# Kernel tuning notes

Measured on AMD Instinct MI355X. Metric: run time of the kernel, lower is better.

Reference implementation:

```python
import jax, jax.numpy as jnp
import numpy as np

N, H, R2, T, E, POS, L = 50000, 256, 460, 3, 100000, 3, 2
RRELU_SLOPE = (1.0 / 8 + 1.0 / 3) / 2  # eval-mode rrelu = leaky with mean slope


def setup_inputs() -> dict:
    key = jax.random.key(0)
    ks = jax.random.split(key, 24)
    s = 0.05
    return {
        'src': jax.random.randint(ks[0], (T, E), 0, N, dtype=jnp.int32),
        'dst': jax.random.randint(ks[1], (T, E), 0, N, dtype=jnp.int32),
        'etype': jax.random.randint(ks[2], (T, E), 0, R2, dtype=jnp.int32),
        'r_to_e': jax.random.randint(ks[3], (T, E), 0, N, dtype=jnp.int32),
        'r_seg': jax.random.randint(ks[4], (T, E), 0, R2, dtype=jnp.int32),
        'pos_enc': jax.random.normal(ks[5], (T, N, POS), jnp.float32),
        'dynamic_emb': jax.random.normal(ks[6], (N, H), jnp.float32),
        'emb_rel': jax.random.normal(ks[7], (R2, H), jnp.float32) * s,
        'gru_W_ih': jax.random.normal(ks[8], (3 * H, 2 * H), jnp.float32) * s,
        'gru_W_hh': jax.random.normal(ks[9], (3 * H, H), jnp.float32) * s,
        'gru_b_ih': jnp.zeros((3 * H,), jnp.float32),
        'gru_b_hh': jnp.zeros((3 * H,), jnp.float32),
        'W_neigh': jax.random.normal(ks[10], (L, H, H), jnp.float32) * s,
        'W_loop': jax.random.normal(ks[11], (L, H, H), jnp.float32) * s,
        'W_evolve': jax.random.normal(ks[12], (L, H, H), jnp.float32) * s,
        'W_hp': jax.random.normal(ks[13], (H, H + POS), jnp.float32) * s,
        'b_hp': jnp.zeros((H,), jnp.float32),
        'W_v': jax.random.normal(ks[14], (H, H), jnp.float32) * s,
        'b_v': jnp.zeros((H,), jnp.float32),
        'W_o': jax.random.normal(ks[15], (H, H), jnp.float32) * s,
        'b_o': jnp.zeros((H,), jnp.float32),
        'time_W': jax.random.normal(ks[16], (H, H), jnp.float32) * s,
        'time_b': jnp.zeros((H,), jnp.float32),
        'glob_W': jax.random.normal(ks[17], (H, H), jnp.float32) * s,
        'glob_b': jnp.zeros((H,), jnp.float32),
    }


def _l2norm(x):
    return x / jnp.maximum(jnp.linalg.norm(x, axis=-1, keepdims=True), 1e-12)


def _gru_cell(x, hprev, W_ih, W_hh, b_ih, b_hh):
    gi = x @ W_ih.T + b_ih
    gh = hprev @ W_hh.T + b_hh
    i_r, i_z, i_n = jnp.split(gi, 3, axis=-1)
    h_r, h_z, h_n = jnp.split(gh, 3, axis=-1)
    r = jax.nn.sigmoid(i_r + h_r)
    z = jax.nn.sigmoid(i_z + h_z)
    n = jnp.tanh(i_n + r * h_n)
    return (1.0 - z) * n + z * hprev


def _forward(src, dst, etype, r_to_e, r_seg, pos_enc, dynamic_emb, emb_rel,
             gru_W_ih, gru_W_hh, gru_b_ih, gru_b_hh,
             W_neigh, W_loop, W_evolve, W_hp, b_hp, W_v, b_v, W_o, b_o,
             time_W, time_b, glob_W, glob_b):
    h = _l2norm(dynamic_emb)  # layer_norm=True path: F.normalize
    h0 = emb_rel
    outs = []
    for t in range(T):  # sequence_len snapshots
        # per-relation mean of involved entity embeddings (r_len/uniq_r spans)
        feat = h[r_to_e[t]]                                   # [E, H]
        sums = jax.ops.segment_sum(feat, r_seg[t], num_segments=R2)
        cnts = jax.ops.segment_sum(jnp.ones((E,), feat.dtype), r_seg[t], num_segments=R2)
        x_mean = jnp.where(cnts[:, None] > 0, sums / jnp.maximum(cnts, 1.0)[:, None], 0.0)
        x_in = jnp.concatenate([emb_rel, x_mean], axis=1)     # [R2, 2H]
        h0 = _l2norm(_gru_cell(x_in, h0, gru_W_ih, gru_W_hh, gru_b_ih, gru_b_hh))
        # UnionRGCN layers: msg = (h_src + rel[etype]) @ W_neigh, sum-agg * 1/in_deg,
        # plus self-loop (loop_weight if in_deg>0 else evolve_loop_weight), rrelu.
        deg = jax.ops.segment_sum(jnp.ones((E,), h.dtype), dst[t], num_segments=N)
        norm = jnp.where(deg > 0, 1.0 / jnp.maximum(deg, 1.0), 0.0)[:, None]
        nh = h
        for l in range(L):
            msg = (nh[src[t]] + h0[etype[t]]) @ W_neigh[l]    # [E, H]
            agg = jax.ops.segment_sum(msg, dst[t], num_segments=N) * norm
            loop = jnp.where(deg[:, None] > 0, nh @ W_loop[l], nh @ W_evolve[l])
            pre = agg + loop
            nh = jnp.where(pre >= 0, pre, RRELU_SLOPE * pre)
        current_h = nh
        # global attention over seq-len-1 -> out_proj(v_proj(x)) in eval mode
        atten_in = jnp.tanh(jnp.concatenate([current_h, pos_enc[t]], axis=1) @ W_hp.T + b_hp)
        global_h = (atten_in @ W_v.T + b_v) @ W_o.T + b_o
        current_h = _l2norm(current_h)
        tw = jax.nn.sigmoid(h @ time_W + time_b)
        h = tw * current_h + (1.0 - tw) * h
        gw = jax.nn.sigmoid(h @ glob_W + glob_b)
        outs.append(gw * global_h + (1.0 - gw) * h)
    return jnp.stack(outs)  # [T, N, H] history_embs


def reference(src, dst, etype, r_to_e, r_seg, pos_enc, dynamic_emb, emb_rel,
              gru_W_ih, gru_W_hh, gru_b_ih, gru_b_hh,
              W_neigh, W_loop, W_evolve, W_hp, b_hp, W_v, b_v, W_o, b_o,
              time_W, time_b, glob_W, glob_b):
    return _forward(src, dst, etype, r_to_e, r_seg, pos_enc, dynamic_emb, emb_rel,
                    gru_W_ih, gru_W_hh, gru_b_ih, gru_b_hh,
                    W_neigh, W_loop, W_evolve, W_hp, b_hp, W_v, b_v, W_o, b_o,
                    time_W, time_b, glob_W, glob_b)
```

## Files before the change

### kernel.cpp

```cpp
#include <hip/hip_runtime.h>
#include <math.h>

#define NN 50000
#define HH 256
#define RR 460
#define TT 3
#define EE 100000
#define PP 3
#define SLOPE 0.22916666666666666f
#define NBIN (RR + NN)
#define NBIN3 (3*NBIN)

typedef __bf16 bf16_t;
typedef bf16_t bf16x8 __attribute__((ext_vector_type(8)));
typedef float f32x4 __attribute__((ext_vector_type(4)));

static const size_t NHf = (size_t)NN * HH;

__device__ __forceinline__ float sigm(float x){ return 1.0f/(1.0f+__expf(-x)); }
__device__ __forceinline__ float leaky(float x){ return (x >= 0.f) ? x : SLOPE*x; }

__device__ __forceinline__ void gload_lds16(const void* g, void* l){
  __builtin_amdgcn_global_load_lds((const __attribute__((address_space(1))) void*)g,
                                   (__attribute__((address_space(3))) void*)l, 16, 0, 0);
}

__global__ __launch_bounds__(256) void tconv_all_k(
    const float* __restrict__ Wn, const float* __restrict__ Wl, const float* __restrict__ We,
    const float* __restrict__ timW, const float* __restrict__ globW,
    bf16_t* __restrict__ bst2, bf16_t* __restrict__ wdT,
    bf16_t* __restrict__ timT, bf16_t* __restrict__ globT){
  int z = blockIdx.z;
  const float* in; const float* in2 = nullptr; bf16_t* outp; int ldout;
  switch(z){
    case 0: in = Wn;           outp = bst2;                       ldout = 512; break;
    case 1: in = Wl;           outp = bst2 + 256;                 ldout = 512; break;
    case 2: in = Wn + 65536;   outp = bst2 + (size_t)256*512;     ldout = 512; break;
    case 3: in = Wl + 65536;   outp = bst2 + (size_t)256*512+256; ldout = 512; break;
    case 4: in = We;          in2 = Wl;         outp = wdT;         ldout = 256; break;
    case 5: in = We + 65536;  in2 = Wl + 65536; outp = wdT + 65536; ldout = 256; break;
    case 6: in = timW;  outp = timT;  ldout = 256; break;
    default:in = globW; outp = globT; ldout = 256; break;
  }
  __shared__ float tile[32][33];
  int n0 = blockIdx.x*32, k0 = blockIdx.y*32;
  int tx = threadIdx.x & 31, ty = threadIdx.x >> 5;
  #pragma unroll
  for (int j=0;j<4;j++){
    size_t idx = (size_t)(k0+ty+j*8)*256 + n0+tx;
    float v = in[idx];
    if (in2) v -= in2[idx];
    tile[ty+j*8][tx] = v;
  }
  __syncthreads();
  #pragma unroll
  for (int j=0;j<4;j++)
    outp[(size_t)(n0+ty+j*8)*ldout + k0+tx] = (bf16_t)tile[tx][ty+j*8];
}

__global__ __launch_bounds__(256) void copyall_k(const float* __restrict__ gW_ih,
    const float* __restrict__ gW_hh, const float* __restrict__ W_hp, const float* __restrict__ emb_rel,
    bf16_t* __restrict__ wihAT, bf16_t* __restrict__ wihBT, bf16_t* __restrict__ whhT,
    bf16_t* __restrict__ whpT, bf16_t* __restrict__ h0b){
  int r = blockIdx.x, c = threadIdx.x, y = blockIdx.y;
  if (y == 0)      wihAT[(size_t)r*256+c] = (bf16_t)gW_ih[(size_t)r*512 + c];
  else if (y == 1) wihBT[(size_t)r*256+c] = (bf16_t)gW_ih[(size_t)r*512 + 256 + c];
  else if (y == 2) whhT[(size_t)r*256+c]  = (bf16_t)gW_hh[(size_t)r*256 + c];
  else if (y == 3){ if (r < 256) whpT[(size_t)r*256+c] = (bf16_t)W_hp[(size_t)r*259 + c]; }
  else            { if (r < RR)  h0b[(size_t)r*256+c]  = (bf16_t)emb_rel[(size_t)r*256 + c]; }
}

__global__ __launch_bounds__(256) void misc_k(const float* __restrict__ W_hp, float* __restrict__ WP,
    const float* __restrict__ W_o, const float* __restrict__ b_v, const float* __restrict__ b_o,
    float* __restrict__ b_ov){
  if (blockIdx.x == 0){
    int j = threadIdx.x;
    #pragma unroll
    for (int p=0;p<PP;p++) WP[p*HH + j] = W_hp[(size_t)j*259 + HH + p];
  } else {
    int n = threadIdx.x;
    float s = b_o[n];
    for (int j=0;j<256;j++) s += W_o[(size_t)n*256+j]*b_v[j];
    b_ov[n] = s;
  }
}

__global__ __launch_bounds__(256) void copy_bfw_k(const float* __restrict__ in, bf16_t* __restrict__ outp){
  int r = blockIdx.x, c = threadIdx.x;
  outp[(size_t)r*HH + c] = (bf16_t)in[(size_t)r*HH + c];
}

__global__ __launch_bounds__(256) void sgemm_k(const float* __restrict__ A, const float* __restrict__ B,
                                               float* __restrict__ C, int M, int N, int K){
  __shared__ float As[16][128];
  __shared__ float Bs[16][64];
  int tid = threadIdx.x;
  int tx = tid & 15, ty = tid >> 4;
  int rowBase = blockIdx.x * 128;
  int colBase = blockIdx.y * 64;
  float acc[8][4];
  #pragma unroll
  for (int i=0;i<8;i++)
    #pragma unroll
    for (int j=0;j<4;j++) acc[i][j]=0.f;
  for (int k0=0;k0<K;k0+=16){
    #pragma unroll
    for (int ss=0; ss<2; ss++){
      int s = tid + ss*256;
      int r = s >> 2;
      int kk = (s & 3)*4;
      float4 v = make_float4(0.f,0.f,0.f,0.f);
      int grow = rowBase + r;
      if (grow < M) v = *(const float4*)(A + (size_t)grow*K + k0 + kk);
      As[kk+0][r]=v.x; As[kk+1][r]=v.y; As[kk+2][r]=v.z; As[kk+3][r]=v.w;
    }
    {
      int r = tid >> 4, cc = (tid & 15)*4;
      float4 v = *(const float4*)(B + (size_t)(k0+r)*N + colBase + cc);
      *(float4*)&Bs[r][cc] = v;
    }
    __syncthreads();
    #pragma unroll
    for (int kk=0;kk<16;kk++){
      float a[8], b[4];
      *(float4*)&a[0] = *(const float4*)&As[kk][ty*8];
      *(float4*)&a[4] = *(const float4*)&As[kk][ty*8+4];
      *(float4*)&b[0] = *(const float4*)&Bs[kk][tx*4];
      #pragma unroll
      for (int i=0;i<8;i++)
        #pragma unroll
        for (int j=0;j<4;j++)
          acc[i][j] = fmaf(a[i], b[j], acc[i][j]);
    }
    __syncthreads();
  }
  #pragma unroll
  for (int i=0;i<8;i++){
    int gr = rowBase + ty*8 + i;
    if (gr >= M) continue;
    float4 v = make_float4(acc[i][0], acc[i][1], acc[i][2], acc[i][3]);
    *(float4*)(C + (size_t)gr*N + colBase + tx*4) = v;
  }
}

template<int EPI, int HASB>
__global__ __launch_bounds__(256) void mgemm_k(
    const bf16_t* __restrict__ A0, const bf16_t* __restrict__ Bt,
    float* __restrict__ C, const float* __restrict__ bias,
    int M, int N, int K, const float* __restrict__ e1){
  __shared__ bf16_t As[128*64];
  __shared__ bf16_t Bs[128*64];
  int tid = threadIdx.x;
  int lane = tid & 63, w = tid >> 6;
  int wm = w >> 1, wn = w & 1;
  int rowBase = blockIdx.x * 128;
  int colBase = blockIdx.y * 128;
  f32x4 acc[4][4] = {};

  int lrow = lane >> 3;
  int p    = lane & 7;
  int arow[4];
  #pragma unroll
  for (int c = 0; c < 4; c++){
    int gr = rowBase + c*32 + w*8 + lrow;
    arow[c] = min(gr, M-1);
  }
  for (int k0 = 0; k0 < K; k0 += 64){
    #pragma unroll
    for (int c = 0; c < 4; c++){
      int r = c*32 + w*8 + lrow;
      int s = p ^ (r & 7);
      gload_lds16(A0 + (size_t)arow[c]*K + k0 + s*8, As + (size_t)(c*32 + w*8)*64);
      int gb = colBase + r;
      gload_lds16(Bt + (size_t)gb*K + k0 + s*8, Bs + (size_t)(c*32 + w*8)*64);
    }
    asm volatile("s_waitcnt vmcnt(0)" ::: "memory");
    __syncthreads();
    #pragma unroll
    for (int kk = 0; kk < 2; kk++){
      bf16x8 af[4], bfr[4];
      int sg = kk*4 + (lane >> 4);
      #pragma unroll
      for (int i = 0; i < 4; i++){
        int r = wm*64 + i*16 + (lane & 15);
        af[i] = *(const bf16x8*)(As + r*64 + (sg ^ (r & 7))*8);
      }
      #pragma unroll
      for (int j = 0; j < 4; j++){
        int rn = wn*64 + j*16 + (lane & 15);
        bfr[j] = *(const bf16x8*)(Bs + rn*64 + (sg ^ (rn & 7))*8);
      }
      #pragma unroll
      for (int i = 0; i < 4; i++)
        #pragma unroll
        for (int j = 0; j < 4; j++)
          acc[i][j] = __builtin_amdgcn_mfma_f32_16x16x32_bf16(af[i], bfr[j], acc[i][j], 0, 0, 0);
    }
    __syncthreads();
  }
  int colv[4]; float bb[4];
  #pragma unroll
  for (int j = 0; j < 4; j++){
    colv[j] = colBase + wn*64 + j*16 + (lane & 15);
    bb[j] = HASB ? bias[colv[j]] : 0.f;
  }
  #pragma unroll
  for (int i = 0; i < 4; i++){
    #pragma unroll
    for (int q = 0; q < 4; q++){
      int grt = rowBase + wm*64 + i*16 + ((lane >> 4) << 2) + q;
      if (grt >= M) continue;
      #pragma unroll
      for (int j = 0; j < 4; j++){
        size_t idx = (size_t)grt*N + colv[j];
        float v = acc[i][j][q] + bb[j];
        if (EPI == 8) v += e1[idx];
        C[idx] = v;
      }
    }
  }
}

template<int EPI, int WF32, int WBF, int HASB, int SPLITA>
__global__ __launch_bounds__(512) void mgemm2_k(
    const bf16_t* __restrict__ A0, const bf16_t* __restrict__ A1,
    const bf16_t* __restrict__ Bt,
    float* __restrict__ C, bf16_t* __restrict__ Cb, const float* __restrict__ bias,
    int M, int K,
    const float* __restrict__ e1, const float* __restrict__ e2,
    const bf16_t* __restrict__ eb, const bf16_t* __restrict__ eb2,
    const int* __restrict__ degp, const int* __restrict__ z, const int* __restrict__ nzp){
  int rowBase = blockIdx.x * 128;
  int nzv = 0;
  if (EPI == 5){
    nzv = nzp[0];
    if (rowBase >= nzv) return;
  }
  __shared__ bf16_t As[128*64];
  __shared__ bf16_t Bs[256*64];
  int tid = threadIdx.x;
  int lane = tid & 63, w = tid >> 6;
  int wm = w >> 2, wn = w & 3;
  f32x4 acc[4][4] = {};

  int lrow8 = lane >> 3;
  int p     = lane & 7;
  int arow[2];
  #pragma unroll
  for (int c = 0; c < 2; c++){
    int r = w*16 + c*8 + lrow8;
    int gr = rowBase + r;
    if (EPI == 5) arow[c] = z[min(gr, nzv-1)];
    else          arow[c] = min(gr, M-1);
  }
  for (int k0 = 0; k0 < K; k0 += 64){
    const bf16_t* Ap; int koff; size_t lda;
    if (SPLITA){ Ap = (k0 < 256) ? A0 : A1; koff = k0 & 255; lda = 256; }
    else       { Ap = A0; koff = k0; lda = (size_t)K; }
    #pragma unroll
    for (int c = 0; c < 2; c++){
      int r = w*16 + c*8 + lrow8;
      int s = p ^ (r & 7);
      gload_lds16(Ap + (size_t)arow[c]*lda + koff + s*8, As + (size_t)(w*16 + c*8)*64);
    }
    #pragma unroll
    for (int c = 0; c < 4; c++){
      int r = w*32 + c*8 + lrow8;
      int s = p ^ (r & 7);
      gload_lds16(Bt + (size_t)r*K + k0 + s*8, Bs + (size_t)(w*32 + c*8)*64);
    }
    asm volatile("s_waitcnt vmcnt(0)" ::: "memory");
    __syncthreads();
    #pragma unroll
    for (int kk = 0; kk < 2; kk++){
      bf16x8 af[4], bfr[4];
      int sg = kk*4 + (lane >> 4);
      #pragma unroll
      for (int i = 0; i < 4; i++){
        int r = wm*64 + i*16 + (lane & 15);
        af[i] = *(const bf16x8*)(As + r*64 + (sg ^ (r & 7))*8);
      }
      #pragma unroll
      for (int j = 0; j < 4; j++){
        int rn = wn*64 + j*16 + (lane & 15);
        bfr[j] = *(const bf16x8*)(Bs + rn*64 + (sg ^ (rn & 7))*8);
      }
      #pragma unroll
      for (int i = 0; i < 4; i++)
        #pragma unroll
        for (int j = 0; j < 4; j++)
          acc[i][j] = __builtin_amdgcn_mfma_f32_16x16x32_bf16(af[i], bfr[j], acc[i][j], 0, 0, 0);
    }
    __syncthreads();
  }
  int colv[4]; float bb[4], wp0[4], wp1[4], wp2[4];
  #pragma unroll
  for (int j = 0; j < 4; j++){
    colv[j] = wn*64 + j*16 + (lane & 15);
    bb[j] = HASB ? bias[colv[j]] : 0.f;
    if (EPI == 2){ wp0[j] = e2[colv[j]]; wp1[j] = e2[256+colv[j]]; wp2[j] = e2[512+colv[j]]; }
  }
  #pragma unroll
  for (int i = 0; i < 4; i++){
    #pragma unroll
    for (int q = 0; q < 4; q++){
      int grt = rowBase + wm*64 + i*16 + ((lane >> 4) << 2) + q;
      if (EPI == 5){ if (grt >= nzv) continue; }
      else         { if (grt >= M) continue; }
      int orow = (EPI == 5) ? z[grt] : grt;
      int dflag = 0;
      if (EPI == 4) dflag = degp[orow];
      float p0=0.f, p1=0.f, p2=0.f;
      if (EPI == 2){ p0 = e1[(size_t)grt*3]; p1 = e1[(size_t)grt*3+1]; p2 = e1[(size_t)grt*3+2]; }
      #pragma unroll
      for (int j = 0; j < 4; j++){
        size_t idx = (size_t)orow*256 + colv[j];
        float v = acc[i][j][q] + bb[j];
        if (EPI == 2) v = tanhf(v + p0*wp0[j] + p1*wp1[j] + p2*wp2[j]);
        if (EPI == 3){
          float g = sigm(v);
          v = g*(float)eb[idx] + (1.f-g)*(float)eb2[idx];
        }
        if (EPI == 4) v = (dflag > 0) ? leaky(v) : v;
        if (EPI == 5){
          float praw = (float)Cb[idx];
          v = leaky(praw + v);
        }
        if (EPI == 7) v = sigm(v);
        if (WF32) C[idx] = v;
        if (WBF)  Cb[idx] = (bf16_t)v;
      }
    }
  }
}

__global__ __launch_bounds__(256) void l2norm_k(const float* __restrict__ in, bf16_t* __restrict__ outb){
  int i = blockIdx.x, c = threadIdx.x;
  size_t idx = (size_t)i*HH + c;
  float v = in[idx];
  float ss = v*v;
  #pragma unroll
  for (int o=32;o;o>>=1) ss += __shfl_down(ss, o);
  __shared__ float red[4];
  if ((threadIdx.x & 63)==0) red[threadIdx.x>>6] = ss;
  __syncthreads();
  float tot = red[0]+red[1]+red[2]+red[3];
  outb[idx] = (bf16_t)(v / fmaxf(sqrtf(tot), 1e-12f));
}

__global__ __launch_bounds__(256) void hist3_k(const int* __restrict__ r_seg, const int* __restrict__ dst,
                                               int* __restrict__ cnt){
  int q = blockIdx.x*256 + threadIdx.x;
  if (q >= 3*2*EE) return;
  int t = q / (2*EE);
  int e = q - t*2*EE;
  if (e < EE) atomicAdd(cnt + t*NBIN + r_seg[(size_t)t*EE + e], 1);
  else        atomicAdd(cnt + t*NBIN + RR + dst[(size_t)t*EE + (e-EE)], 1);
}

__global__ __launch_bounds__(1024) void scan1_k(const int* __restrict__ cnt, int* __restrict__ start,
                                                int* __restrict__ bsum, int n){
  __shared__ int s[1024];
  int t = blockIdx.x*1024 + threadIdx.x;
  int v = (t < n) ? cnt[t] : 0;
  s[threadIdx.x] = v;
  __syncthreads();
  for (int off = 1; off < 1024; off <<= 1){
    int x = (threadIdx.x >= off) ? s[threadIdx.x - off] : 0;
    __syncthreads();
    s[threadIdx.x] += x;
    __syncthreads();
  }
  if (t < n) start[t] = s[threadIdx.x] - v;
  if (threadIdx.x == 1023) bsum[blockIdx.x] = s[1023];
}
__global__ __launch_bounds__(256) void scan2_k(const int* __restrict__ bsum, int* __restrict__ boff,
                                               int* __restrict__ start, int nb, int n){
  __shared__ int s[256];
  int t = threadIdx.x;
  int v = (t < nb) ? bsum[t] : 0;
  s[t] = v;
  __syncthreads();
  for (int off = 1; off < 256; off <<= 1){
    int x = (t >= off) ? s[t-off] : 0;
    __syncthreads();
    s[t] += x;
    __syncthreads();
  }
  if (t < nb) boff[t] = s[t] - v;
  if (t == 255) start[n] = s[255];
}
__global__ __launch_bounds__(1024) void scan3_k(int* __restrict__ start, int* __restrict__ cur,
                                                const int* __restrict__ boff, int n){
  int t = blockIdx.x*1024 + threadIdx.x;
  if (t < n){
    int v = start[t] + boff[blockIdx.x];
    start[t] = v;
    cur[t] = v;
  }
}

__global__ __launch_bounds__(256) void fill3_k(const int* __restrict__ r_seg, const int* __restrict__ r_to_e,
    const int* __restrict__ dst, const int* __restrict__ src, const int* __restrict__ ety,
    int* __restrict__ cur, int* __restrict__ rnode, unsigned* __restrict__ dpack){
  int q = blockIdx.x*256 + threadIdx.x;
  if (q >= 3*2*EE) return;
  int t = q / (2*EE);
  int e = q - t*2*EE;
  if (e < EE){
    size_t ge = (size_t)t*EE + e;
    int pp = atomicAdd(cur + t*NBIN + r_seg[ge], 1);
    rnode[pp - EE*t] = r_to_e[ge];
  } else {
    size_t ge = (size_t)t*EE + (e - EE);
    int pp = atomicAdd(cur + t*NBIN + RR + dst[ge], 1);
    dpack[pp - EE*(t+1)] = (unsigned)src[ge] | ((unsigned)ety[ge] << 16);
  }
}

__global__ __launch_bounds__(256) void compact3_k(const int* __restrict__ cnt, int* __restrict__ zAll,
                                                  int* __restrict__ nz){
  int q = blockIdx.x*256 + threadIdx.x;
  int lane = threadIdx.x & 63;
  bool valid = q < 3*NN;
  int qc = valid ? q : 3*NN - 1;
  int t = qc / NN, d = qc - t*NN;
  bool pred = valid && (cnt[t*NBIN + RR + d] == 0);
  int tA = __shfl(t, 0), tB = __shfl(t, 63);
  if (tA == tB){
    unsigned long long m = __ballot(pred);
    int total = __popcll(m);
    int base = 0;
    if (lane == 0 && total > 0) base = atomicAdd(nz + tA, total);
    base = __shfl(base, 0);
    if (pred){
      int myoff = __popcll(m & ((1ULL << lane) - 1ULL));
      zAll[(size_t)tA*NN + base + myoff] = d;
    }
  } else {
    if (pred){
      int pp = atomicAdd(nz + t, 1);
      zAll[(size_t)t*NN + pp] = d;
    }
  }
}

__global__ __launch_bounds__(256) void rmean_k(const int* __restrict__ startT, const int* __restrict__ rnode,
    const bf16_t* __restrict__ hb, bf16_t* __restrict__ meanb, int rbase){
  int r = blockIdx.x, c = threadIdx.x;
  int s0 = startT[r] - rbase, s1 = startT[r+1] - rbase;
  float acc = 0.f, acc2 = 0.f;
  int i = s0;
  for (; i + 1 < s1; i += 2){
    acc  += (float)hb[(size_t)rnode[i]*HH + c];
    acc2 += (float)hb[(size_t)rnode[i+1]*HH + c];
  }
  if (i < s1) acc += (float)hb[(size_t)rnode[i]*HH + c];
  acc += acc2;
  int cnt = s1 - s0;
  meanb[(size_t)r*HH + c] = (bf16_t)((cnt > 0) ? acc/(float)cnt : 0.f);
}

__global__ __launch_bounds__(256) void gru_gate_k(const float* __restrict__ gi,
    const float* __restrict__ ghb, float* __restrict__ h0, bf16_t* __restrict__ h0b){
  int r = blockIdx.x, c = threadIdx.x;
  float ir = gi[(size_t)r*768 + c],       hr = ghb[(size_t)r*768 + c];
  float iz = gi[(size_t)r*768 + 256 + c], hz = ghb[(size_t)r*768 + 256 + c];
  float in_ = gi[(size_t)r*768 + 512 + c], hn = ghb[(size_t)r*768 + 512 + c];
  float rg = sigm(ir + hr);
  float z  = sigm(iz + hz);
  float n  = tanhf(in_ + rg*hn);
  float hp = h0[(size_t)r*HH + c];
  float v = (1.f - z)*n + z*hp;
  float ss = v*v;
  #pragma unroll
  for (int o=32;o;o>>=1) ss += __shfl_down(ss, o);
  __shared__ float red[4];
  if ((threadIdx.x & 63)==0) red[threadIdx.x>>6] = ss;
  __syncthreads();
  float tot = red[0]+red[1]+red[2]+red[3];
  float nv = v / fmaxf(sqrtf(tot), 1e-12f);
  h0[(size_t)r*HH + c] = nv;
  h0b[(size_t)r*HH + c] = (bf16_t)nv;
}

__global__ __launch_bounds__(256) void gatherM_k(const bf16_t* __restrict__ nin,
    const bf16_t* __restrict__ h0b, const int* __restrict__ startT,
    const unsigned* __restrict__ dpack, bf16_t* __restrict__ Amean, int ebase){
  int w = threadIdx.x >> 6, ln = threadIdx.x & 63;
  int d = blockIdx.x*4 + w;
  if (d >= NN) return;
  int s0 = startT[RR + d] - ebase, s1 = startT[RR + d + 1] - ebase;
  int deg = s1 - s0;
  float a0=0.f, a1=0.f, a2=0.f, a3=0.f;
  for (int i = s0; i < s1; i++){
    unsigned se = dpack[i];
    int s = (int)(se & 0xffffu);
    int r = (int)(se >> 16);
    uint2 ra = *(const uint2*)(nin + (size_t)s*HH + ln*4);
    uint2 rb = *(const uint2*)(h0b + (size_t)r*HH + ln*4);
    a0 += __uint_as_float((ra.x & 0xffffu) << 16) + __uint_as_float((rb.x & 0xffffu) << 16);
    a1 += __uint_as_float(ra.x & 0xffff0000u)     + __uint_as_float(rb.x & 0xffff0000u);
    a2 += __uint_as_float((ra.y & 0xffffu) << 16) + __uint_as_float((rb.y & 0xffffu) << 16);
    a3 += __uint_as_float(ra.y & 0xffff0000u)     + __uint_as_float(rb.y & 0xffff0000u);
  }
  float inv = (deg > 0) ? 1.f/(float)deg : 0.f;
  bf16_t m[4] = { (bf16_t)(a0*inv), (bf16_t)(a1*inv), (bf16_t)(a2*inv), (bf16_t)(a3*inv) };
  *(uint2*)(Amean + (size_t)d*HH + ln*4) = *(const uint2*)m;
}

__global__ __launch_bounds__(256) void l2up_k(const bf16_t* __restrict__ nh2b, const bf16_t* __restrict__ sg,
    bf16_t* __restrict__ hb){
  int i = blockIdx.x, c = threadIdx.x;
  size_t idx = (size_t)i*HH + c;
  float v = (float)nh2b[idx];
  float ss = v*v;
  #pragma unroll
  for (int o=32;o;o>>=1) ss += __shfl_down(ss, o);
  __shared__ float red[4];
  if ((threadIdx.x & 63)==0) red[threadIdx.x>>6] = ss;
  __syncthreads();
  float tot = red[0]+red[1]+red[2]+red[3];
  float curn = v / fmaxf(sqrtf(tot), 1e-12f);
  float s = (float)sg[idx];
  float hn = s*curn + (1.f-s)*(float)hb[idx];
  hb[idx] = (bf16_t)hn;
}

extern "C" void kernel_launch(void* const* d_in, const int* in_sizes, int n_in,
                              void* d_out, int out_size, void* d_ws, size_t ws_size,
                              hipStream_t stream) {
  const int*   src     = (const int*)  d_in[0];
  const int*   dst     = (const int*)  d_in[1];
  const int*   etype   = (const int*)  d_in[2];
  const int*   r_to_e  = (const int*)  d_in[3];
  const int*   r_seg   = (const int*)  d_in[4];
  const float* pos_enc = (const float*)d_in[5];
  const float* dyn_emb = (const float*)d_in[6];
  const float* emb_rel = (const float*)d_in[7];
  const float* gW_ih   = (const float*)d_in[8];
  const float* gW_hh   = (const float*)d_in[9];
  const float* gb_ih   = (const float*)d_in[10];
  const float* gb_hh   = (const float*)d_in[11];
  const float* W_neigh = (const float*)d_in[12];
  const float* W_loop  = (const float*)d_in[13];
  const float* W_evolve= (const float*)d_in[14];
  const float* W_hp    = (const float*)d_in[15];
  const float* b_hp    = (const float*)d_in[16];
  const float* W_v     = (const float*)d_in[17];
  const float* b_v     = (const float*)d_in[18];
  const float* W_o     = (const float*)d_in[19];
  const float* b_o     = (const float*)d_in[20];
  const float* time_W  = (const float*)d_in[21];
  const float* time_b  = (const float*)d_in[22];
  const float* glob_W  = (const float*)d_in[23];
  const float* glob_b  = (const float*)d_in[24];
  float* out = (float*)d_out;
  (void)in_sizes; (void)n_in; (void)out_size; (void)ws_size;

  char* ws = (char*)d_ws;
  size_t off = 0;
  auto allocB = [&](size_t bytes)->char*{
    char* pp = ws + off; off += (bytes + 255) & ~(size_t)255;
    return pp;
  };
  float*  tmp    = (float*) allocB(NHf*4);
  bf16_t* h_bf   = (bf16_t*)allocB(NHf*2);
  bf16_t* nh_bf  = (bf16_t*)allocB(NHf*2);
  bf16_t* nh2_bf = (bf16_t*)allocB(NHf*2);
  bf16_t* gh_bf  = (bf16_t*)allocB(NHf*2);
  bf16_t* Amean  = (bf16_t*)tmp;
  bf16_t* sgate  = (bf16_t*)(tmp + NHf/2);
  bf16_t* attn_bf= nh_bf;

  float*  h0    = (float*) allocB((size_t)RR*HH*4);
  bf16_t* h0b   = (bf16_t*)allocB((size_t)RR*HH*2);
  bf16_t* meanb = (bf16_t*)allocB((size_t)RR*HH*2);
  float*  gi0   = (float*) allocB((size_t)RR*768*4);
  float*  gi    = (float*) allocB((size_t)RR*768*4);
  float*  ghb   = (float*) allocB((size_t)RR*768*4);
  bf16_t* wihAT = (bf16_t*)allocB((size_t)768*256*2);
  bf16_t* wihBT = (bf16_t*)allocB((size_t)768*256*2);
  bf16_t* whhT  = (bf16_t*)allocB((size_t)768*256*2);
  float*  WP    = (float*) allocB((size_t)PP*HH*4);
  float*  WovF  = (float*) allocB((size_t)HH*HH*4);
  float*  b_ov  = (float*) allocB((size_t)HH*4);
  bf16_t* bst2  = (bf16_t*)allocB((size_t)2*HH*512*2);
  bf16_t* wdT   = (bf16_t*)allocB((size_t)2*HH*HH*2);
  bf16_t* whpT  = (bf16_t*)allocB((size_t)HH*HH*2);
  bf16_t* wovT  = (bf16_t*)allocB((size_t)HH*HH*2);
  bf16_t* timT  = (bf16_t*)allocB((size_t)HH*HH*2);
  bf16_t* globT = (bf16_t*)allocB((size_t)HH*HH*2);
  int* cnt    = (int*)allocB((size_t)(NBIN3+4)*4);
  int* start  = (int*)allocB((size_t)(NBIN3+1)*4);
  int* cur    = (int*)allocB((size_t)NBIN3*4);
  int* rnode  = (int*)allocB((size_t)3*EE*4);
  unsigned* dpack = (unsigned*)allocB((size_t)3*EE*4);
  int* zAll   = (int*)allocB((size_t)3*NN*4);
  int* bsum   = (int*)allocB(256*4);
  int* boff   = (int*)allocB(256*4);
  int* nz     = cnt + NBIN3;

  const int MT  = (NN + 127)/128;
  const int NB3 = (NBIN3 + 1023)/1024;

  copyall_k<<<dim3(768,5), 256, 0, stream>>>(gW_ih, gW_hh, W_hp, emb_rel,
                                             wihAT, wihBT, whhT, whpT, h0b);
  tconv_all_k<<<dim3(8,8,8), 256, 0, stream>>>(W_neigh, W_loop, W_evolve, time_W, glob_W,
                                               bst2, wdT, timT, globT);
  misc_k<<<2, 256, 0, stream>>>(W_hp, WP, W_o, b_v, b_o, b_ov);
  sgemm_k<<<dim3(2,4), 256, 0, stream>>>(W_o, W_v, WovF, 256, 256, 256);
  copy_bfw_k<<<HH, 256, 0, stream>>>(WovF, wovT);
  l2norm_k<<<NN, 256, 0, stream>>>(dyn_emb, h_bf);
  hipMemcpyAsync(h0, emb_rel, (size_t)RR*HH*4, hipMemcpyDeviceToDevice, stream);
  mgemm_k<0,1><<<dim3(4,6), 256, 0, stream>>>(h0b, wihAT, gi0, gb_ih, RR, 768, 256, nullptr);

  hipMemsetAsync(cnt, 0, (size_t)(NBIN3+4)*4, stream);
  hist3_k<<<(6*EE+255)/256, 256, 0, stream>>>(r_seg, dst, cnt);
  scan1_k<<<NB3, 1024, 0, stream>>>(cnt, start, bsum, NBIN3);
  scan2_k<<<1, 256, 0, stream>>>(bsum, boff, start, NB3, NBIN3);
  scan3_k<<<NB3, 1024, 0, stream>>>(start, cur, boff, NBIN3);
  fill3_k<<<(6*EE+255)/256, 256, 0, stream>>>(r_seg, r_to_e, dst, src, etype, cur, rnode, dpack);
  compact3_k<<<(3*NN+255)/256, 256, 0, stream>>>(cnt, zAll, nz);

  for (int t=0; t<TT; t++){
    const float* posT = pos_enc + (size_t)t*NN*PP;
    const int* startT = start + (size_t)t*NBIN;
    const int* degT   = cnt + (size_t)t*NBIN + RR;
    const int* zT     = zAll + (size_t)t*NN;
    const int* nzT    = nz + t;

    rmean_k<<<RR, 256, 0, stream>>>(startT, rnode, h_bf, meanb, EE*t);
    mgemm_k<8,0><<<dim3(4,6), 256, 0, stream>>>(meanb, wihBT, gi, nullptr, RR, 768, 256, gi0);
    mgemm_k<0,1><<<dim3(4,6), 256, 0, stream>>>(h0b, whhT, ghb, gb_hh, RR, 768, 256, nullptr);
    gru_gate_k<<<RR, 256, 0, stream>>>(gi, ghb, h0, h0b);

    gatherM_k<<<(NN+3)/4, 256, 0, stream>>>(h_bf, h0b, startT, dpack, Amean, EE*(t+1));
    mgemm2_k<4,0,1,0,1><<<MT, 512, 0, stream>>>(Amean, h_bf, bst2, nullptr, nh_bf, nullptr,
        NN, 512, nullptr, nullptr, nullptr, nullptr, degT, nullptr, nullptr);
    mgemm2_k<5,0,1,0,0><<<MT, 512, 0, stream>>>(h_bf, nullptr, wdT, nullptr, nh_bf, nullptr,
        NN, 256, nullptr, nullptr, nullptr, nullptr, nullptr, zT, nzT);

    gatherM_k<<<(NN+3)/4, 256, 0, stream>>>(nh_bf, h0b, startT, dpack, Amean, EE*(t+1));
    mgemm2_k<4,0,1,0,1><<<MT, 512, 0, stream>>>(Amean, nh_bf, bst2 + (size_t)HH*512, nullptr, nh2_bf, nullptr,
        NN, 512, nullptr, nullptr, nullptr, nullptr, degT, nullptr, nullptr);
    mgemm2_k<5,0,1,0,0><<<MT, 512, 0, stream>>>(nh_bf, nullptr, wdT + (size_t)HH*HH, nullptr, nh2_bf, nullptr,
        NN, 256, nullptr, nullptr, nullptr, nullptr, nullptr, zT, nzT);

    mgemm2_k<2,0,1,1,0><<<MT, 512, 0, stream>>>(nh2_bf, nullptr, whpT, nullptr, attn_bf, b_hp,
        NN, 256, posT, WP, nullptr, nullptr, nullptr, nullptr, nullptr);
    mgemm2_k<0,0,1,1,0><<<MT, 512, 0, stream>>>(attn_bf, nullptr, wovT, nullptr, gh_bf, b_ov,
        NN, 256, nullptr, nullptr, nullptr, nullptr, nullptr, nullptr, nullptr);

    mgemm2_k<7,0,1,1,0><<<MT, 512, 0, stream>>>(h_bf, nullptr, timT, nullptr, sgate, time_b,
        NN, 256, nullptr, nullptr, nullptr, nullptr, nullptr, nullptr, nullptr);
    l2up_k<<<NN, 256, 0, stream>>>(nh2_bf, sgate, h_bf);
    mgemm2_k<3,1,0,1,0><<<MT, 512, 0, stream>>>(h_bf, nullptr, globT, out + (size_t)t*NHf, nullptr, glob_b,
        NN, 256, nullptr, nullptr, gh_bf, h_bf, nullptr, nullptr, nullptr);
  }
}
```

Measured before the change: 1.370 ms.

## Halve GEMM row tile to 64 and unroll gather loop by two

New measurement: 1.329 ms. 3.0% less time.

```diff
diff --git a/kernel.cpp b/kernel.cpp
--- a/kernel.cpp
+++ b/kernel.cpp
@@ -222,7 +222,7 @@
 }
 
 template<int EPI, int WF32, int WBF, int HASB, int SPLITA>
-__global__ __launch_bounds__(512) void mgemm2_k(
+__global__ __launch_bounds__(512, 6) void mgemm2_k(
     const bf16_t* __restrict__ A0, const bf16_t* __restrict__ A1,
     const bf16_t* __restrict__ Bt,
     float* __restrict__ C, bf16_t* __restrict__ Cb, const float* __restrict__ bias,
@@ -230,38 +230,35 @@
     const float* __restrict__ e1, const float* __restrict__ e2,
     const bf16_t* __restrict__ eb, const bf16_t* __restrict__ eb2,
     const int* __restrict__ degp, const int* __restrict__ z, const int* __restrict__ nzp){
-  int rowBase = blockIdx.x * 128;
+  int rowBase = blockIdx.x * 64;
   int nzv = 0;
   if (EPI == 5){
     nzv = nzp[0];
     if (rowBase >= nzv) return;
   }
-  __shared__ bf16_t As[128*64];
+  __shared__ bf16_t As[64*64];
   __shared__ bf16_t Bs[256*64];
   int tid = threadIdx.x;
   int lane = tid & 63, w = tid >> 6;
-  int wm = w >> 2, wn = w & 3;
-  f32x4 acc[4][4] = {};
+  f32x4 acc[4][2] = {};
 
   int lrow8 = lane >> 3;
   int p     = lane & 7;
-  int arow[2];
-  #pragma unroll
-  for (int c = 0; c < 2; c++){
-    int r = w*16 + c*8 + lrow8;
+  int arow;
+  {
+    int r = w*8 + lrow8;
     int gr = rowBase + r;
-    if (EPI == 5) arow[c] = z[min(gr, nzv-1)];
-    else          arow[c] = min(gr, M-1);
+    if (EPI == 5) arow = z[min(gr, nzv-1)];
+    else          arow = min(gr, M-1);
   }
   for (int k0 = 0; k0 < K; k0 += 64){
     const bf16_t* Ap; int koff; size_t lda;
     if (SPLITA){ Ap = (k0 < 256) ? A0 : A1; koff = k0 & 255; lda = 256; }
     else       { Ap = A0; koff = k0; lda = (size_t)K; }
-    #pragma unroll
-    for (int c = 0; c < 2; c++){
-      int r = w*16 + c*8 + lrow8;
+    {
+      int r = w*8 + lrow8;
       int s = p ^ (r & 7);
-      gload_lds16(Ap + (size_t)arow[c]*lda + koff + s*8, As + (size_t)(w*16 + c*8)*64);
+      gload_lds16(Ap + (size_t)arow*lda + koff + s*8, As + (size_t)(w*8)*64);
     }
     #pragma unroll
     for (int c = 0; c < 4; c++){
@@ -273,30 +270,30 @@
     __syncthreads();
     #pragma unroll
     for (int kk = 0; kk < 2; kk++){
-      bf16x8 af[4], bfr[4];
+      bf16x8 af[4], bfr[2];
       int sg = kk*4 + (lane >> 4);
       #pragma unroll
       for (int i = 0; i < 4; i++){
-        int r = wm*64 + i*16 + (lane & 15);
+        int r = i*16 + (lane & 15);
         af[i] = *(const bf16x8*)(As + r*64 + (sg ^ (r & 7))*8);
       }
       #pragma unroll
-      for (int j = 0; j < 4; j++){
-        int rn = wn*64 + j*16 + (lane & 15);
+      for (int j = 0; j < 2; j++){
+        int rn = w*32 + j*16 + (lane & 15);
         bfr[j] = *(const bf16x8*)(Bs + rn*64 + (sg ^ (rn & 7))*8);
       }
       #pragma unroll
       for (int i = 0; i < 4; i++)
         #pragma unroll
-        for (int j = 0; j < 4; j++)
+        for (int j = 0; j < 2; j++)
           acc[i][j] = __builtin_amdgcn_mfma_f32_16x16x32_bf16(af[i], bfr[j], acc[i][j], 0, 0, 0);
     }
     __syncthreads();
   }
-  int colv[4]; float bb[4], wp0[4], wp1[4], wp2[4];
-  #pragma unroll
-  for (int j = 0; j < 4; j++){
-    colv[j] = wn*64 + j*16 + (lane & 15);
+  int colv[2]; float bb[2], wp0[2], wp1[2], wp2[2];
+  #pragma unroll
+  for (int j = 0; j < 2; j++){
+    colv[j] = w*32 + j*16 + (lane & 15);
     bb[j] = HASB ? bias[colv[j]] : 0.f;
     if (EPI == 2){ wp0[j] = e2[colv[j]]; wp1[j] = e2[256+colv[j]]; wp2[j] = e2[512+colv[j]]; }
   }
@@ -304,7 +301,7 @@
   for (int i = 0; i < 4; i++){
     #pragma unroll
     for (int q = 0; q < 4; q++){
-      int grt = rowBase + wm*64 + i*16 + ((lane >> 4) << 2) + q;
+      int grt = rowBase + i*16 + ((lane >> 4) << 2) + q;
       if (EPI == 5){ if (grt >= nzv) continue; }
       else         { if (grt >= M) continue; }
       int orow = (EPI == 5) ? z[grt] : grt;
@@ -313,7 +310,7 @@
       float p0=0.f, p1=0.f, p2=0.f;
       if (EPI == 2){ p0 = e1[(size_t)grt*3]; p1 = e1[(size_t)grt*3+1]; p2 = e1[(size_t)grt*3+2]; }
       #pragma unroll
-      for (int j = 0; j < 4; j++){
+      for (int j = 0; j < 2; j++){
         size_t idx = (size_t)orow*256 + colv[j];
         float v = acc[i][j][q] + bb[j];
         if (EPI == 2) v = tanhf(v + p0*wp0[j] + p1*wp1[j] + p2*wp2[j]);
@@ -493,12 +490,26 @@
   int s0 = startT[RR + d] - ebase, s1 = startT[RR + d + 1] - ebase;
   int deg = s1 - s0;
   float a0=0.f, a1=0.f, a2=0.f, a3=0.f;
-  for (int i = s0; i < s1; i++){
+  int i = s0;
+  for (; i + 1 < s1; i += 2){
+    unsigned seA = dpack[i], seB = dpack[i+1];
+    uint2 raA = *(const uint2*)(nin + (size_t)(seA & 0xffffu)*HH + ln*4);
+    uint2 raB = *(const uint2*)(nin + (size_t)(seB & 0xffffu)*HH + ln*4);
+    uint2 rbA = *(const uint2*)(h0b + (size_t)(seA >> 16)*HH + ln*4);
+    uint2 rbB = *(const uint2*)(h0b + (size_t)(seB >> 16)*HH + ln*4);
+    a0 += __uint_as_float((raA.x & 0xffffu) << 16) + __uint_as_float((rbA.x & 0xffffu) << 16)
+        + __uint_as_float((raB.x & 0xffffu) << 16) + __uint_as_float((rbB.x & 0xffffu) << 16);
+    a1 += __uint_as_float(raA.x & 0xffff0000u)     + __uint_as_float(rbA.x & 0xffff0000u)
+        + __uint_as_float(raB.x & 0xffff0000u)     + __uint_as_float(rbB.x & 0xffff0000u);
+    a2 += __uint_as_float((raA.y & 0xffffu) << 16) + __uint_as_float((rbA.y & 0xffffu) << 16)
+        + __uint_as_float((raB.y & 0xffffu) << 16) + __uint_as_float((rbB.y & 0xffffu) << 16);
+    a3 += __uint_as_float(raA.y & 0xffff0000u)     + __uint_as_float(rbA.y & 0xffff0000u)
+        + __uint_as_float(raB.y & 0xffff0000u)     + __uint_as_float(rbB.y & 0xffff0000u);
+  }
+  if (i < s1){
     unsigned se = dpack[i];
-    int s = (int)(se & 0xffffu);
-    int r = (int)(se >> 16);
-    uint2 ra = *(const uint2*)(nin + (size_t)s*HH + ln*4);
-    uint2 rb = *(const uint2*)(h0b + (size_t)r*HH + ln*4);
+    uint2 ra = *(const uint2*)(nin + (size_t)(se & 0xffffu)*HH + ln*4);
+    uint2 rb = *(const uint2*)(h0b + (size_t)(se >> 16)*HH + ln*4);
     a0 += __uint_as_float((ra.x & 0xffffu) << 16) + __uint_as_float((rb.x & 0xffffu) << 16);
     a1 += __uint_as_float(ra.x & 0xffff0000u)     + __uint_as_float(rb.x & 0xffff0000u);
     a2 += __uint_as_float((ra.y & 0xffffu) << 16) + __uint_as_float((rb.y & 0xffffu) << 16);
@@ -601,7 +612,7 @@
   int* boff   = (int*)allocB(256*4);
   int* nz     = cnt + NBIN3;
 
-  const int MT  = (NN + 127)/128;
+  const int MT2 = (NN + 63)/64;
   const int NB3 = (NBIN3 + 1023)/1024;
 
   copyall_k<<<dim3(768,5), 256, 0, stream>>>(gW_ih, gW_hh, W_hp, emb_rel,
@@ -636,26 +647,26 @@
     gru_gate_k<<<RR, 256, 0, stream>>>(gi, ghb, h0, h0b);
 
     gatherM_k<<<(NN+3)/4, 256, 0, stream>>>(h_bf, h0b, startT, dpack, Amean, EE*(t+1));
-    mgemm2_k<4,0,1,0,1><<<MT, 512, 0, stream>>>(Amean, h_bf, bst2, nullptr, nh_bf, nullptr,
+    mgemm2_k<4,0,1,0,1><<<MT2, 512, 0, stream>>>(Amean, h_bf, bst2, nullptr, nh_bf, nullptr,
         NN, 512, nullptr, nullptr, nullptr, nullptr, degT, nullptr, nullptr);
-    mgemm2_k<5,0,1,0,0><<<MT, 512, 0, stream>>>(h_bf, nullptr, wdT, nullptr, nh_bf, nullptr,
+    mgemm2_k<5,0,1,0,0><<<MT2, 512, 0, stream>>>(h_bf, nullptr, wdT, nullptr, nh_bf, nullptr,
         NN, 256, nullptr, nullptr, nullptr, nullptr, nullptr, zT, nzT);
 
     gatherM_k<<<(NN+3)/4, 256, 0, stream>>>(nh_bf, h0b, startT, dpack, Amean, EE*(t+1));
-    mgemm2_k<4,0,1,0,1><<<MT, 512, 0, stream>>>(Amean, nh_bf, bst2 + (size_t)HH*512, nullptr, nh2_bf, nullptr,
+    mgemm2_k<4,0,1,0,1><<<MT2, 512, 0, stream>>>(Amean, nh_bf, bst2 + (size_t)HH*512, nullptr, nh2_bf, nullptr,
         NN, 512, nullptr, nullptr, nullptr, nullptr, degT, nullptr, nullptr);
-    mgemm2_k<5,0,1,0,0><<<MT, 512, 0, stream>>>(nh_bf, nullptr, wdT + (size_t)HH*HH, nullptr, nh2_bf, nullptr,
+    mgemm2_k<5,0,1,0,0><<<MT2, 512, 0, stream>>>(nh_bf, nullptr, wdT + (size_t)HH*HH, nullptr, nh2_bf, nullptr,
         NN, 256, nullptr, nullptr, nullptr, nullptr, nullptr, zT, nzT);
 
-    mgemm2_k<2,0,1,1,0><<<MT, 512, 0, stream>>>(nh2_bf, nullptr, whpT, nullptr, attn_bf, b_hp,
+    mgemm2_k<2,0,1,1,0><<<MT2, 512, 0, stream>>>(nh2_bf, nullptr, whpT, nullptr, attn_bf, b_hp,
         NN, 256, posT, WP, nullptr, nullptr, nullptr, nullptr, nullptr);
-    mgemm2_k<0,0,1,1,0><<<MT, 512, 0, stream>>>(attn_bf, nullptr, wovT, nullptr, gh_bf, b_ov,
+    mgemm2_k<0,0,1,1,0><<<MT2, 512, 0, stream>>>(attn_bf, nullptr, wovT, nullptr, gh_bf, b_ov,
         NN, 256, nullptr, nullptr, nullptr, nullptr, nullptr, nullptr, nullptr);
 
-    mgemm2_k<7,0,1,1,0><<<MT, 512, 0, stream>>>(h_bf, nullptr, timT, nullptr, sgate, time_b,
+    mgemm2_k<7,0,1,1,0><<<MT2, 512, 0, stream>>>(h_bf, nullptr, timT, nullptr, sgate, time_b,
         NN, 256, nullptr, nullptr, nullptr, nullptr, nullptr, nullptr, nullptr);
     l2up_k<<<NN, 256, 0, stream>>>(nh2_bf, sgate, h_bf);
-    mgemm2_k<3,1,0,1,0><<<MT, 512, 0, stream>>>(h_bf, nullptr, globT, out + (size_t)t*NHf, nullptr, glob_b,
+    mgemm2_k<3,1,0,1,0><<<MT2, 512, 0, stream>>>(h_bf, nullptr, globT, out + (size_t)t*NHf, nullptr, glob_b,
         NN, 256, nullptr, nullptr, gh_bf, h_bf, nullptr, nullptr, nullptr);
   }
 }
```
